# Kernel optimization log

Hardware: AMD Instinct MI355X
Metric: run time of the kernel (lower is better)

## Reference

```python
import jax, jax.numpy as jnp
import numpy as np

D = 512   # dim (number of groups)
H = 8192  # h = dim * v
U = 64    # u
V = H // D  # 16
N = 4096  # batch
EPS = 1e-12  # torch F.normalize eps


def setup_inputs() -> dict:
    key = jax.random.key(0)
    k_x, k_w1, k_b1, k_w2, k_b2 = jax.random.split(key, 5)
    x = jax.random.normal(k_x, (N, H), dtype=jnp.float32)
    # grouped Conv1d(dim*v, dim*u, k=1, groups=dim) == per-group [u, v] matmul
    s1 = 1.0 / np.sqrt(V)
    W1 = jax.random.uniform(k_w1, (D, U, V), jnp.float32, -s1, s1)
    b1 = jax.random.uniform(k_b1, (D, U), jnp.float32, -s1, s1)
    # grouped Conv1d(dim*u, dim, k=1, groups=dim) == per-group [1, u] matmul
    s2 = 1.0 / np.sqrt(U)
    W2 = jax.random.uniform(k_w2, (D, U), jnp.float32, -s2, s2)
    b2 = jax.random.uniform(k_b2, (D,), jnp.float32, -s2, s2)
    return {"x": x, "W1": W1, "b1": b1, "W2": W2, "b2": b2}


def reference(x, W1, b1, W2, b2):
    # x: [N, H] -> [N, D, V] (channel layout of Conv1d groups)
    xg = x.reshape(-1, D, V)
    # grouped 1x1 conv #1: per-group v -> u matmul, + bias
    h1 = jnp.einsum('ndv,duv->ndu', xg, W1) + b1  # [N, D, U]
    h1 = jax.nn.elu(h1)
    # grouped 1x1 conv #2: per-group u -> 1 matmul, + bias
    y = jnp.einsum('ndu,du->nd', h1, W2) + b2  # [N, D]
    # L2 normalize (torch F.normalize semantics: x / max(||x||, eps))
    nrm = jnp.sqrt(jnp.sum(y * y, axis=-1, keepdims=True))
    return y / jnp.maximum(nrm, EPS)
```

## Files before the change

### kernel.cpp

```cpp
#include <hip/hip_runtime.h>
#include <math.h>

#define D_ 512
#define H_ 8192
#define U_ 64
#define V_ 16
#define N_ 4096

#define ROWS_PER_WAVE 256
#define NB_N (N_ / ROWS_PER_WAVE)
#define TILES (ROWS_PER_WAVE / 16)

typedef __bf16 bf16x8 __attribute__((ext_vector_type(8)));
typedef float f32x4 __attribute__((ext_vector_type(4)));

__global__ __launch_bounds__(256) void k1_div_encoder(
        const float* __restrict__ x,
        const float* __restrict__ W1,
        const float* __restrict__ b1,
        const float* __restrict__ W2,
        const float* __restrict__ b2,
        float* __restrict__ y) {
    const int tid  = threadIdx.x;
    const int lane = tid & 63;
    const int wave = __builtin_amdgcn_readfirstlane(tid >> 6);
    const int q    = lane >> 4;
    const int m    = lane & 15;

    const int dblk = blockIdx.x & 127;
    const int nblk = blockIdx.x >> 7;
    const int d  = dblk * 4 + wave;
    const int r0 = nblk * ROWS_PER_WAVE;

    const int vbase = (q & 1) * 8;

    bf16x8 Afrag[4];
    #pragma unroll
    for (int c = 0; c < 4; ++c) {
        const float* wp = W1 + ((size_t)d * U_ + c * 16 + m) * V_ + vbase;
        f32x4 w0 = *(const f32x4*)wp;
        f32x4 w1v = *(const f32x4*)(wp + 4);
        float wf[8] = {w0.x, w0.y, w0.z, w0.w, w1v.x, w1v.y, w1v.z, w1v.w};
        bf16x8 a;
        if (q < 2) {
            #pragma unroll
            for (int i = 0; i < 8; ++i) a[i] = (__bf16)wf[i];
        } else {
            #pragma unroll
            for (int i = 0; i < 8; ++i) {
                __bf16 h = (__bf16)wf[i];
                a[i] = (__bf16)(wf[i] - (float)h);
            }
        }
        Afrag[c] = a;
    }

    f32x4 b1frag[4], w2frag[4];
    #pragma unroll
    for (int c = 0; c < 4; ++c) {
        b1frag[c] = *(const f32x4*)(b1 + (size_t)d * U_ + c * 16 + q * 4);
        w2frag[c] = *(const f32x4*)(W2 + (size_t)d * U_ + c * 16 + q * 4);
    }
    const float b2s = b2[d];

    for (int t = 0; t < TILES; ++t) {
        const int row = r0 + t * 16 + m;
        const float* xp = x + (size_t)row * H_ + d * V_ + vbase;
        f32x4 x0 = *(const f32x4*)xp;
        f32x4 x1 = *(const f32x4*)(xp + 4);
        float xf[8] = {x0.x, x0.y, x0.z, x0.w, x1.x, x1.y, x1.z, x1.w};

        bf16x8 bhi, blo;
        #pragma unroll
        for (int i = 0; i < 8; ++i) {
            __bf16 h = (__bf16)xf[i];
            bhi[i] = h;
            blo[i] = (__bf16)(xf[i] - (float)h);
        }

        float partial = 0.0f;
        #pragma unroll
        for (int c = 0; c < 4; ++c) {
            f32x4 acc = b1frag[c];
            acc = __builtin_amdgcn_mfma_f32_16x16x32_bf16(Afrag[c], bhi, acc, 0, 0, 0);
            acc = __builtin_amdgcn_mfma_f32_16x16x32_bf16(Afrag[c], blo, acc, 0, 0, 0);
            #pragma unroll
            for (int r = 0; r < 4; ++r) {
                float h = acc[r];
                float e = (h > 0.0f) ? h : (__expf(h) - 1.0f);
                partial = fmaf(w2frag[c][r], e, partial);
            }
        }
        partial += __shfl_xor(partial, 16, 64);
        partial += __shfl_xor(partial, 32, 64);
        if (q == 0) {
            y[(size_t)(r0 + t * 16 + m) * D_ + d] = partial + b2s;
        }
    }
}

__global__ __launch_bounds__(256) void k2_l2_normalize(float* __restrict__ y) {
    const int n = blockIdx.x;
    const int t = threadIdx.x;
    float* row = y + (size_t)n * D_;

    float v0 = row[t];
    float v1 = row[t + 256];
    float ss = v0 * v0 + v1 * v1;

    #pragma unroll
    for (int off = 32; off > 0; off >>= 1) {
        ss += __shfl_down(ss, off, 64);
    }

    __shared__ float wsum[4];
    if ((t & 63) == 0) wsum[t >> 6] = ss;
    __syncthreads();
    const float tot = wsum[0] + wsum[1] + wsum[2] + wsum[3];

    const float scale = 1.0f / fmaxf(sqrtf(tot), 1e-12f);

    row[t]       = v0 * scale;
    row[t + 256] = v1 * scale;
}

extern "C" void kernel_launch(void* const* d_in, const int* in_sizes, int n_in,
                              void* d_out, int out_size, void* d_ws, size_t ws_size,
                              hipStream_t stream) {
    const float* x  = (const float*)d_in[0];
    const float* W1 = (const float*)d_in[1];
    const float* b1 = (const float*)d_in[2];
    const float* W2 = (const float*)d_in[3];
    const float* b2 = (const float*)d_in[4];
    float* y = (float*)d_out;

    k1_div_encoder<<<dim3(NB_N * (D_ / 4)), dim3(256), 0, stream>>>(
        x, W1, b1, W2, b2, y);
    k2_l2_normalize<<<dim3(N_), dim3(256), 0, stream>>>(y);
}
```

Measured before the change: 239.2 us.

## Stage x tiles through shared memory with coalesced loads and batched y stores

Changes the encoder kernel from one wave per group streaming 256 rows to blocks covering a 32-row by 16-group tile. The tile of x is loaded into LDS with fully coalesced 1KB-per-row vector loads, and outputs are gathered in LDS and written as float4. This replaces the old strided 64-byte per-row x reads and scattered scalar y stores. The cost is that W1, b1 and W2 are now reloaded and re-split to bf16 by many more blocks, plus extra LDS traffic and barriers.

```diff
diff --git a/kernel.cpp b/kernel.cpp
--- a/kernel.cpp
+++ b/kernel.cpp
@@ -7,9 +7,10 @@
 #define V_ 16
 #define N_ 4096
 
-#define ROWS_PER_WAVE 256
-#define NB_N (N_ / ROWS_PER_WAVE)
-#define TILES (ROWS_PER_WAVE / 16)
+#define BR 32
+#define BG 16
+#define XPAD 4
+#define XSTR (BG * V_ + XPAD)
 
 typedef __bf16 bf16x8 __attribute__((ext_vector_type(8)));
 typedef float f32x4 __attribute__((ext_vector_type(4)));
@@ -21,81 +22,111 @@
         const float* __restrict__ W2,
         const float* __restrict__ b2,
         float* __restrict__ y) {
+    __shared__ float xs[BR][XSTR];
+    __shared__ float ytile[BR][BG + 1];
+
     const int tid  = threadIdx.x;
     const int lane = tid & 63;
     const int wave = __builtin_amdgcn_readfirstlane(tid >> 6);
     const int q    = lane >> 4;
     const int m    = lane & 15;
-
-    const int dblk = blockIdx.x & 127;
-    const int nblk = blockIdx.x >> 7;
-    const int d  = dblk * 4 + wave;
-    const int r0 = nblk * ROWS_PER_WAVE;
-
     const int vbase = (q & 1) * 8;
 
-    bf16x8 Afrag[4];
-    #pragma unroll
-    for (int c = 0; c < 4; ++c) {
-        const float* wp = W1 + ((size_t)d * U_ + c * 16 + m) * V_ + vbase;
-        f32x4 w0 = *(const f32x4*)wp;
-        f32x4 w1v = *(const f32x4*)(wp + 4);
-        float wf[8] = {w0.x, w0.y, w0.z, w0.w, w1v.x, w1v.y, w1v.z, w1v.w};
-        bf16x8 a;
-        if (q < 2) {
-            #pragma unroll
-            for (int i = 0; i < 8; ++i) a[i] = (__bf16)wf[i];
-        } else {
+    const int nb = blockIdx.x & 127;
+    const int db = blockIdx.x >> 7;
+    const int r0 = nb * BR;
+    const int d0 = db * BG;
+
+    {
+        const float* xg = x + (size_t)r0 * H_ + (size_t)d0 * V_;
+        #pragma unroll
+        for (int i = 0; i < 8; ++i) {
+            const int flat = tid + i * 256;
+            const int row  = flat >> 6;
+            const int c4   = flat & 63;
+            f32x4 v = *(const f32x4*)(xg + (size_t)row * H_ + c4 * 4);
+            *(f32x4*)&xs[row][c4 * 4] = v;
+        }
+    }
+    __syncthreads();
+
+    for (int gi = 0; gi < 4; ++gi) {
+        const int gl = wave * 4 + gi;
+        const int d  = d0 + gl;
+
+        bf16x8 Afrag[4];
+        #pragma unroll
+        for (int c = 0; c < 4; ++c) {
+            const float* wp = W1 + ((size_t)d * U_ + c * 16 + m) * V_ + vbase;
+            f32x4 w0 = *(const f32x4*)wp;
+            f32x4 w1v = *(const f32x4*)(wp + 4);
+            float wf[8] = {w0.x, w0.y, w0.z, w0.w, w1v.x, w1v.y, w1v.z, w1v.w};
+            bf16x8 a;
+            if (q < 2) {
+                #pragma unroll
+                for (int i = 0; i < 8; ++i) a[i] = (__bf16)wf[i];
+            } else {
+                #pragma unroll
+                for (int i = 0; i < 8; ++i) {
+                    __bf16 h = (__bf16)wf[i];
+                    a[i] = (__bf16)(wf[i] - (float)h);
+                }
+            }
+            Afrag[c] = a;
+        }
+        f32x4 b1frag[4], w2frag[4];
+        #pragma unroll
+        for (int c = 0; c < 4; ++c) {
+            b1frag[c] = *(const f32x4*)(b1 + (size_t)d * U_ + c * 16 + q * 4);
+            w2frag[c] = *(const f32x4*)(W2 + (size_t)d * U_ + c * 16 + q * 4);
+        }
+        const float b2s = b2[d];
+
+        #pragma unroll
+        for (int t = 0; t < 2; ++t) {
+            const float* bp = &xs[t * 16 + m][gl * V_ + vbase];
+            f32x4 x0 = *(const f32x4*)bp;
+            f32x4 x1 = *(const f32x4*)(bp + 4);
+            float xf[8] = {x0.x, x0.y, x0.z, x0.w, x1.x, x1.y, x1.z, x1.w};
+            bf16x8 bhi, blo;
             #pragma unroll
             for (int i = 0; i < 8; ++i) {
-                __bf16 h = (__bf16)wf[i];
-                a[i] = (__bf16)(wf[i] - (float)h);
+                __bf16 h = (__bf16)xf[i];
+                bhi[i] = h;
+                blo[i] = (__bf16)(xf[i] - (float)h);
+            }
+
+            float partial = 0.0f;
+            #pragma unroll
+            for (int c = 0; c < 4; ++c) {
+                f32x4 acc = b1frag[c];
+                acc = __builtin_amdgcn_mfma_f32_16x16x32_bf16(Afrag[c], bhi, acc, 0, 0, 0);
+                acc = __builtin_amdgcn_mfma_f32_16x16x32_bf16(Afrag[c], blo, acc, 0, 0, 0);
+                #pragma unroll
+                for (int r = 0; r < 4; ++r) {
+                    float h = acc[r];
+                    float e = (h > 0.0f) ? h : (__expf(h) - 1.0f);
+                    partial = fmaf(w2frag[c][r], e, partial);
+                }
+            }
+            partial += __shfl_xor(partial, 16, 64);
+            partial += __shfl_xor(partial, 32, 64);
+            if (q == 0) {
+                ytile[t * 16 + m][gl] = partial + b2s;
             }
         }
-        Afrag[c] = a;
     }
+    __syncthreads();
 
-    f32x4 b1frag[4], w2frag[4];
-    #pragma unroll
-    for (int c = 0; c < 4; ++c) {
-        b1frag[c] = *(const f32x4*)(b1 + (size_t)d * U_ + c * 16 + q * 4);
-        w2frag[c] = *(const f32x4*)(W2 + (size_t)d * U_ + c * 16 + q * 4);
-    }
-    const float b2s = b2[d];
-
-    for (int t = 0; t < TILES; ++t) {
-        const int row = r0 + t * 16 + m;
-        const float* xp = x + (size_t)row * H_ + d * V_ + vbase;
-        f32x4 x0 = *(const f32x4*)xp;
-        f32x4 x1 = *(const f32x4*)(xp + 4);
-        float xf[8] = {x0.x, x0.y, x0.z, x0.w, x1.x, x1.y, x1.z, x1.w};
-
-        bf16x8 bhi, blo;
-        #pragma unroll
-        for (int i = 0; i < 8; ++i) {
-            __bf16 h = (__bf16)xf[i];
-            bhi[i] = h;
-            blo[i] = (__bf16)(xf[i] - (float)h);
-        }
-
-        float partial = 0.0f;
-        #pragma unroll
-        for (int c = 0; c < 4; ++c) {
-            f32x4 acc = b1frag[c];
-            acc = __builtin_amdgcn_mfma_f32_16x16x32_bf16(Afrag[c], bhi, acc, 0, 0, 0);
-            acc = __builtin_amdgcn_mfma_f32_16x16x32_bf16(Afrag[c], blo, acc, 0, 0, 0);
-            #pragma unroll
-            for (int r = 0; r < 4; ++r) {
-                float h = acc[r];
-                float e = (h > 0.0f) ? h : (__expf(h) - 1.0f);
-                partial = fmaf(w2frag[c][r], e, partial);
-            }
-        }
-        partial += __shfl_xor(partial, 16, 64);
-        partial += __shfl_xor(partial, 32, 64);
-        if (q == 0) {
-            y[(size_t)(r0 + t * 16 + m) * D_ + d] = partial + b2s;
-        }
+    if (tid < 128) {
+        const int row = tid >> 2;
+        const int c4  = (tid & 3) * 4;
+        f32x4 v;
+        v.x = ytile[row][c4 + 0];
+        v.y = ytile[row][c4 + 1];
+        v.z = ytile[row][c4 + 2];
+        v.w = ytile[row][c4 + 3];
+        *(f32x4*)(y + (size_t)(r0 + row) * D_ + d0 + c4) = v;
     }
 }
 
@@ -134,7 +165,7 @@
     const float* b2 = (const float*)d_in[4];
     float* y = (float*)d_out;
 
-    k1_div_encoder<<<dim3(NB_N * (D_ / 4)), dim3(256), 0, stream>>>(
+    k1_div_encoder<<<dim3((N_ / BR) * (D_ / BG)), dim3(256), 0, stream>>>(
         x, W1, b1, W2, b2, y);
     k2_l2_normalize<<<dim3(N_), dim3(256), 0, stream>>>(y);
 }
```

After: 256.3 us. 7.1% more time.
